# Performance work log

Measured on AMD Instinct MI355X. Metric: run time of the kernel, lower is better.

The kernel has to match this reference:

```python
import jax, jax.numpy as jnp
import numpy as np

N_ATOMS = 10000
N_PAIR = 100000
F = 128
N_HEAD = 4
FH = F // N_HEAD  # 32
DEGREES = [1, 2, 3]
N_DEG = len(DEGREES)
REPEATS = np.array([2 * l + 1 for l in DEGREES])  # [3,5,7]
M_TOT = int(REPEATS.sum())  # 15
K_RBF = 32


def ssp(x):
    # shifted softplus: softplus(x) - log(2)
    return jax.nn.softplus(x) - jnp.log(2.0).astype(x.dtype)


def setup_inputs() -> dict:
    key = jax.random.key(0)
    ks = jax.random.split(key, 16)
    inp = {
        "x": jax.random.normal(ks[0], (N_ATOMS, F), jnp.float32),
        "rbf_ij": jax.random.normal(ks[1], (N_PAIR, K_RBF), jnp.float32),
        "sph_ij": jax.random.normal(ks[2], (N_PAIR, M_TOT), jnp.float32),
        "phi_r_cut": jax.random.uniform(ks[3], (N_PAIR,), jnp.float32),
        "idx_i": jnp.sort(jax.random.randint(ks[4], (N_PAIR,), 0, N_ATOMS)),
        "idx_j": jax.random.randint(ks[5], (N_PAIR,), 0, N_ATOMS),
        "pair_mask": jnp.ones((N_PAIR,), jnp.float32),
        # params
        "W_Q": jax.random.normal(ks[6], (N_DEG, N_HEAD, FH, FH), jnp.float32) / np.sqrt(FH),
        "W_K": jax.random.normal(ks[7], (N_DEG, N_HEAD, FH, FH), jnp.float32) / np.sqrt(FH),
        # in2f MLP: single dense F -> F
        "W_in": jax.random.normal(ks[8], (F, F), jnp.float32) / np.sqrt(F),
        "b_in": jnp.zeros((F,), jnp.float32),
        # radial filter MLP: K -> K (ssp) -> n_deg*F
        "W_f1": jax.random.normal(ks[9], (K_RBF, K_RBF), jnp.float32) / np.sqrt(K_RBF),
        "b_f1": jnp.zeros((K_RBF,), jnp.float32),
        "W_f2": jax.random.normal(ks[10], (K_RBF, N_DEG * F), jnp.float32) / np.sqrt(K_RBF),
        "b_f2": jnp.zeros((N_DEG * F,), jnp.float32),
        # f2out MLP: single dense F -> F
        "W_out": jax.random.normal(ks[11], (F, F), jnp.float32) / np.sqrt(F),
        "b_out": jnp.zeros((F,), jnp.float32),
    }
    return inp


def reference(x, rbf_ij, sph_ij, phi_r_cut, idx_i, idx_j, pair_mask,
              W_Q, W_K, W_in, b_in, W_f1, b_f1, W_f2, b_f2, W_out, b_out):
    n = x.shape[0]
    # in2f embedding (last in2f dim == F)
    x_f = x @ W_in + b_in                                  # (n, F)
    x_head = x_f.reshape(n, N_HEAD, FH)                    # (n, h, FH)

    # per-degree, per-head linear maps (the nested vmap matmuls)
    Q = jnp.einsum('dhij,nhj->ndhi', W_Q, x_head)          # (n, n_deg, h, FH)
    K = jnp.einsum('dhij,nhj->ndhi', W_K, x_head)

    m = pair_mask[:, None, None, None]
    Q_i = Q[idx_i] * m                                     # (P, n_deg, h, FH)
    K_j = K[idx_j] * m

    # radial filter: MLP(rbf) -> (P, n_deg, h, FH), scaled by cutoff
    h1 = ssp(rbf_ij @ W_f1 + b_f1)
    W_ij = (h1 @ W_f2 + b_f2).reshape(-1, N_DEG, N_HEAD, FH)
    W_ij = W_ij * phi_r_cut[:, None, None, None]

    # attention coefficients per degree/head
    alpha = jnp.sum(Q_i * K_j * W_ij, axis=-1)             # (P, n_deg, h)
    alpha = jnp.repeat(alpha, repeats=REPEATS, axis=1, total_repeat_length=M_TOT)  # (P, m_tot, h)
    alpha = alpha / jnp.sqrt(jnp.asarray(FH, x.dtype))     # att_scale

    # outer product of neighbor features with spherical harmonics
    x_j = x_head[idx_j] * pair_mask[:, None, None]         # (P, h, FH)
    z_ij = jnp.einsum('pm,phf->pmhf', sph_ij, x_j)         # (P, m_tot, h, FH)
    z_ij = alpha[:, :, :, None] * z_ij
    z_ij = z_ij.reshape(z_ij.shape[0], M_TOT, F)           # (P, m_tot, F)

    agg = jax.ops.segment_sum(z_ij, idx_i, num_segments=n)  # (n, m_tot, F)

    # f2out projection (last f2out dim == F)
    out = agg @ W_out + b_out                               # (n, m_tot, F)
    return out
```

## Files before the change

kernel.cpp:

```cpp
#include <hip/hip_runtime.h>
#include <hip/hip_bf16.h>

#define N_ATOMS 10000
#define N_PAIR  100000
#define F_DIM   128
#define N_HEAD  4
#define FH      32
#define N_DEG   3
#define M_TOT   15
#define K_RBF   32
#define R_OUT   (N_ATOMS * M_TOT)
#define PPB     50

typedef __attribute__((ext_vector_type(8))) short short8;
typedef __attribute__((ext_vector_type(4))) float f32x4;

union frag_cast { int i[4]; short8 s; };

__device__ __forceinline__ float sspf(float v) {
    float sp = fmaxf(v, 0.f) + log1pf(expf(-fabsf(v)));
    return sp - 0.69314718055994531f;
}

__device__ __forceinline__ unsigned short bf16_rne(float x) {
    unsigned int u = __float_as_uint(x);
    unsigned int r = u + 0x7fffu + ((u >> 16) & 1u);
    return (unsigned short)(r >> 16);
}
__device__ __forceinline__ float bf16_tof(unsigned short h) {
    return __uint_as_float(((unsigned int)h) << 16);
}

__global__ __launch_bounds__(256) void k_binit(
    const float* __restrict__ b, float4* __restrict__ out, int n4)
{
    int i = blockIdx.x * 256 + threadIdx.x;
    int stride = gridDim.x * 256;
    for (; i < n4; i += stride) {
        int c4 = i & 31;
        out[i] = *(const float4*)(b + c4 * 4);
    }
}

__global__ __launch_bounds__(256) void k_gemm128(
    const float* __restrict__ A, const float* __restrict__ B,
    const float* __restrict__ bias, float* __restrict__ C, int rows)
{
    __shared__ float As[32][132];
    __shared__ float Bs[32][132];
    int r0 = blockIdx.x * 128;
    int t = threadIdx.x;
    int ty = t >> 4, tx = t & 15;

    float acc[8][8];
    #pragma unroll
    for (int i = 0; i < 8; ++i)
        #pragma unroll
        for (int j = 0; j < 8; ++j) acc[i][j] = 0.f;

    for (int k0 = 0; k0 < 128; k0 += 32) {
        #pragma unroll
        for (int r = 0; r < 16; ++r) {
            int idx = t + 256 * r;
            int row = idx >> 5, kk = idx & 31;
            int grow = r0 + row;
            As[kk][row] = (grow < rows) ? A[grow * 128 + k0 + kk] : 0.f;
        }
        #pragma unroll
        for (int r = 0; r < 16; ++r) {
            int idx = t + 256 * r;
            int kk = idx >> 7, c = idx & 127;
            Bs[kk][c] = B[(k0 + kk) * 128 + c];
        }
        __syncthreads();

        #pragma unroll
        for (int kk = 0; kk < 32; ++kk) {
            float a[8], b[8];
            *(float4*)&a[0] = *(const float4*)&As[kk][ty * 4];
            *(float4*)&a[4] = *(const float4*)&As[kk][64 + ty * 4];
            *(float4*)&b[0] = *(const float4*)&Bs[kk][tx * 4];
            *(float4*)&b[4] = *(const float4*)&Bs[kk][64 + tx * 4];
            #pragma unroll
            for (int i = 0; i < 8; ++i)
                #pragma unroll
                for (int j = 0; j < 8; ++j)
                    acc[i][j] = fmaf(a[i], b[j], acc[i][j]);
        }
        __syncthreads();
    }

    float bj[8];
    #pragma unroll
    for (int j = 0; j < 4; ++j) { bj[j] = bias[tx * 4 + j]; bj[4 + j] = bias[64 + tx * 4 + j]; }

    #pragma unroll
    for (int i = 0; i < 8; ++i) {
        int row = r0 + ((i < 4) ? (ty * 4 + i) : (64 + ty * 4 + (i - 4)));
        if (row < rows) {
            float4 v0, v1;
            v0.x = acc[i][0] + bj[0]; v0.y = acc[i][1] + bj[1];
            v0.z = acc[i][2] + bj[2]; v0.w = acc[i][3] + bj[3];
            v1.x = acc[i][4] + bj[4]; v1.y = acc[i][5] + bj[5];
            v1.z = acc[i][6] + bj[6]; v1.w = acc[i][7] + bj[7];
            *(float4*)&C[row * 128 + tx * 4] = v0;
            *(float4*)&C[row * 128 + 64 + tx * 4] = v1;
        }
    }
}

__global__ __launch_bounds__(384) void k_qk(
    const float* __restrict__ xh, const float* __restrict__ W_Q,
    const float* __restrict__ W_K, float* __restrict__ Q, float* __restrict__ K)
{
    __shared__ float xfs[32][128];
    int t = threadIdx.x;
    int h = (t >> 5) & 3;
    float wq[32], wk[32];
    const float4* wqp = (const float4*)(W_Q + t * 32);
    const float4* wkp = (const float4*)(W_K + t * 32);
    #pragma unroll
    for (int j4 = 0; j4 < 8; ++j4) {
        float4 a = wqp[j4], b = wkp[j4];
        wq[4 * j4 + 0] = a.x; wq[4 * j4 + 1] = a.y; wq[4 * j4 + 2] = a.z; wq[4 * j4 + 3] = a.w;
        wk[4 * j4 + 0] = b.x; wk[4 * j4 + 1] = b.y; wk[4 * j4 + 2] = b.z; wk[4 * j4 + 3] = b.w;
    }
    int ab = blockIdx.x * 32;
    for (int idx = t; idx < 4096; idx += 384) {
        int aa = idx >> 7, f = idx & 127;
        int ag = ab + aa;
        xfs[aa][f] = (ag < N_ATOMS) ? xh[ag * 128 + f] : 0.f;
    }
    __syncthreads();
    for (int aa = 0; aa < 32; ++aa) {
        int ag = ab + aa;
        if (ag >= N_ATOMS) break;
        const float4* xv = (const float4*)&xfs[aa][h * 32];
        float q0 = 0.f, q1 = 0.f, k0 = 0.f, k1 = 0.f;
        #pragma unroll
        for (int j4 = 0; j4 < 8; j4 += 2) {
            float4 x0 = xv[j4], x1 = xv[j4 + 1];
            q0 = fmaf(wq[4 * j4 + 0], x0.x, q0); q0 = fmaf(wq[4 * j4 + 1], x0.y, q0);
            q0 = fmaf(wq[4 * j4 + 2], x0.z, q0); q0 = fmaf(wq[4 * j4 + 3], x0.w, q0);
            q1 = fmaf(wq[4 * j4 + 4], x1.x, q1); q1 = fmaf(wq[4 * j4 + 5], x1.y, q1);
            q1 = fmaf(wq[4 * j4 + 6], x1.z, q1); q1 = fmaf(wq[4 * j4 + 7], x1.w, q1);
            k0 = fmaf(wk[4 * j4 + 0], x0.x, k0); k0 = fmaf(wk[4 * j4 + 1], x0.y, k0);
            k0 = fmaf(wk[4 * j4 + 2], x0.z, k0); k0 = fmaf(wk[4 * j4 + 3], x0.w, k0);
            k1 = fmaf(wk[4 * j4 + 4], x1.x, k1); k1 = fmaf(wk[4 * j4 + 5], x1.y, k1);
            k1 = fmaf(wk[4 * j4 + 6], x1.z, k1); k1 = fmaf(wk[4 * j4 + 7], x1.w, k1);
        }
        Q[ag * 384 + t] = q0 + q1;
        K[ag * 384 + t] = k0 + k1;
    }
}

__global__ __launch_bounds__(256) void k_cvt_w2(
    const float* __restrict__ W, unsigned short* __restrict__ Wh,
    unsigned short* __restrict__ Wl)
{
    int idx = blockIdx.x * 256 + threadIdx.x;
    if (idx < 12288) {
        int e = idx >> 5, k = idx & 31;
        float v = W[k * 384 + e];
        unsigned short h = bf16_rne(v);
        unsigned short l = bf16_rne(v - bf16_tof(h));
        Wh[e * 32 + k] = h;
        Wl[e * 32 + k] = l;
    }
}

__global__ __launch_bounds__(256) void k_pair(
    const float* __restrict__ rbf, const float* __restrict__ phi,
    const float* __restrict__ mask, const int* __restrict__ idx_i,
    const int* __restrict__ idx_j, const float* __restrict__ W_f1,
    const float* __restrict__ b_f1, const unsigned short* __restrict__ W2h,
    const unsigned short* __restrict__ W2l, const float* __restrict__ b_f2,
    const float* __restrict__ Q, const float* __restrict__ K,
    float* __restrict__ alpha)
{
    __shared__ float g_s[16][388];
    __shared__ unsigned int h1p_s[16][36];
    __shared__ int   i_s[16];
    __shared__ int   j_s[16];
    __shared__ float phim_s[16];

    float (*rbf_s)[33] = (float (*)[33])(&g_s[0][0]);
    float (*wf1_s)[33] = (float (*)[33])(&g_s[0][0] + 16 * 33);

    int t = threadIdx.x;
    int p0 = blockIdx.x * 16;

    for (int idx = t; idx < 1536; idx += 256) {
        if (idx < 512) {
            rbf_s[idx >> 5][idx & 31] = rbf[p0 * 32 + idx];
        } else {
            int k = idx - 512;
            wf1_s[k >> 5][k & 31] = W_f1[k];
        }
    }
    if (t < 16) {
        int pg = p0 + t;
        i_s[t] = idx_i[pg];
        j_s[t] = idx_j[pg];
        float m = mask[pg];
        phim_s[t] = phi[pg] * m * m * 0.17677669529663687f;
    }
    __syncthreads();

    {
        int p = t >> 4, c0 = (t & 15) * 2;
        float acc0 = b_f1[c0], acc1 = b_f1[c0 + 1];
        #pragma unroll
        for (int k = 0; k < 32; ++k) {
            float rv = rbf_s[p][k];
            acc0 = fmaf(rv, wf1_s[k][c0], acc0);
            acc1 = fmaf(rv, wf1_s[k][c0 + 1], acc1);
        }
        float h0 = sspf(acc0), h1v = sspf(acc1);
        unsigned short hh0 = bf16_rne(h0);
        unsigned short ll0 = bf16_rne(h0 - bf16_tof(hh0));
        unsigned short hh1 = bf16_rne(h1v);
        unsigned short ll1 = bf16_rne(h1v - bf16_tof(hh1));
        h1p_s[p][c0]     = ((unsigned int)hh0 << 16) | (unsigned int)ll0;
        h1p_s[p][c0 + 1] = ((unsigned int)hh1 << 16) | (unsigned int)ll1;
    }
    __syncthreads();

    #pragma unroll
    for (int it = 0; it < 6; ++it) {
        int idx = it * 256 + t;
        int p = idx / 96;
        int c4 = idx - p * 96;
        const float4* qp = (const float4*)(Q + i_s[p] * 384) + c4;
        const float4* kp = (const float4*)(K + j_s[p] * 384) + c4;
        float4 qv = *qp, kv = *kp;
        float4 gv;
        gv.x = qv.x * kv.x; gv.y = qv.y * kv.y;
        gv.z = qv.z * kv.z; gv.w = qv.w * kv.w;
        *(float4*)&g_s[p][c4 * 4] = gv;
    }
    __syncthreads();

    int wave = t >> 6, lane = t & 63;
    int quad = lane >> 4, l15 = lane & 15;

    short8 ah, al;
    {
        const unsigned int* hp = &h1p_s[l15][quad * 8];
        uint4 u01 = *(const uint4*)hp;
        uint4 u23 = *(const uint4*)(hp + 4);
        unsigned int u[8] = {u01.x, u01.y, u01.z, u01.w, u23.x, u23.y, u23.z, u23.w};
        frag_cast fh, fl;
        #pragma unroll
        for (int q = 0; q < 4; ++q) {
            unsigned int a0 = u[2 * q], a1 = u[2 * q + 1];
            fh.i[q] = (int)((a0 >> 16) | (a1 & 0xffff0000u));
            fl.i[q] = (int)((a0 & 0xffffu) | (a1 << 16));
        }
        ah = fh.s;
        al = fl.s;
    }

    #pragma unroll
    for (int dd = 0; dd < 3; ++dd) {
        int dh = wave * 3 + dd;
        int e_base = dh * 32;
        short8 bh0 = *(const short8*)(W2h + (e_base + l15) * 32 + quad * 8);
        short8 bl0 = *(const short8*)(W2l + (e_base + l15) * 32 + quad * 8);
        short8 bh1 = *(const short8*)(W2h + (e_base + 16 + l15) * 32 + quad * 8);
        short8 bl1 = *(const short8*)(W2l + (e_base + 16 + l15) * 32 + quad * 8);
        float b2v0 = b_f2[e_base + l15];
        float b2v1 = b_f2[e_base + 16 + l15];

        f32x4 s0 = {0.f, 0.f, 0.f, 0.f};
        f32x4 s1 = {0.f, 0.f, 0.f, 0.f};
        s0 = __builtin_amdgcn_mfma_f32_16x16x32_bf16(ah, bh0, s0, 0, 0, 0);
        s1 = __builtin_amdgcn_mfma_f32_16x16x32_bf16(ah, bh1, s1, 0, 0, 0);
        s0 = __builtin_amdgcn_mfma_f32_16x16x32_bf16(al, bh0, s0, 0, 0, 0);
        s1 = __builtin_amdgcn_mfma_f32_16x16x32_bf16(al, bh1, s1, 0, 0, 0);
        s0 = __builtin_amdgcn_mfma_f32_16x16x32_bf16(ah, bl0, s0, 0, 0, 0);
        s1 = __builtin_amdgcn_mfma_f32_16x16x32_bf16(ah, bl1, s1, 0, 0, 0);

        float vsum[4];
        #pragma unroll
        for (int r = 0; r < 4; ++r) {
            int prow = quad * 4 + r;
            float v = (s0[r] + b2v0) * g_s[prow][e_base + l15]
                    + (s1[r] + b2v1) * g_s[prow][e_base + 16 + l15];
            #pragma unroll
            for (int off = 8; off >= 1; off >>= 1)
                v += __shfl_xor(v, off, 16);
            vsum[r] = v;
        }
        if (l15 == 0) {
            #pragma unroll
            for (int r = 0; r < 4; ++r) {
                int prow = quad * 4 + r;
                alpha[(p0 + prow) * 12 + dh] = vsum[r] * phim_s[prow];
            }
        }
    }
}

__global__ __launch_bounds__(256) void k_xw(
    const float* __restrict__ xh, const float* __restrict__ W,
    float* __restrict__ xwh)
{
    __shared__ float xs[32][132];
    int t = threadIdx.x;
    int a0 = blockIdx.x * 32;
    #pragma unroll
    for (int it = 0; it < 4; ++it) {
        int idx = t + it * 256;
        int row = idx >> 5, c4 = (idx & 31) * 4;
        int ga = a0 + row;
        float4 v = make_float4(0.f, 0.f, 0.f, 0.f);
        if (ga < N_ATOMS) v = *(const float4*)(xh + ga * 128 + c4);
        *(float4*)&xs[row][c4] = v;
    }
    __syncthreads();

    int c = t & 127;
    int half = t >> 7;
    #pragma unroll
    for (int h = 0; h < 4; ++h) {
        float w[32];
        #pragma unroll
        for (int k = 0; k < 32; ++k) w[k] = W[(h * 32 + k) * 128 + c];
        float acc[16];
        #pragma unroll
        for (int i = 0; i < 16; ++i) acc[i] = 0.f;
        #pragma unroll
        for (int k = 0; k < 32; ++k) {
            float wv = w[k];
            #pragma unroll
            for (int i = 0; i < 16; ++i)
                acc[i] = fmaf(xs[half * 16 + i][h * 32 + k], wv, acc[i]);
        }
        #pragma unroll
        for (int i = 0; i < 16; ++i) {
            int ga = a0 + half * 16 + i;
            if (ga < N_ATOMS) xwh[(long)ga * 512 + h * 128 + c] = acc[i];
        }
    }
}

__device__ __forceinline__ void flush_acc(float* __restrict__ out, int a,
                                          const float* acc, float bout,
                                          int t, bool interior)
{
    float* base = out + (long)a * (M_TOT * 128) + t;
    if (interior) {
        #pragma unroll
        for (int m = 0; m < M_TOT; ++m) base[m * 128] = acc[m] + bout;
    } else {
        #pragma unroll
        for (int m = 0; m < M_TOT; ++m) atomicAdd(&base[m * 128], acc[m]);
    }
}

__global__ __launch_bounds__(512) void k_aggc(
    const float* __restrict__ xwh, const float* __restrict__ alpha,
    const float* __restrict__ sph, const int* __restrict__ idx_i,
    const int* __restrict__ idx_j, const float* __restrict__ mask,
    const float* __restrict__ b_out, float* __restrict__ out)
{
    int tid = threadIdx.x;
    int grp = tid >> 7;
    int t   = tid & 127;
    int g0  = (blockIdx.x * 4 + grp) * PPB;
    int g1  = g0 + PPB;

    float bout = b_out[t];
    int prevA = (g0 > 0) ? idx_i[g0 - 1] : -1;
    int nextA = (g1 < N_PAIR) ? idx_i[g1] : -1;

    float acc[M_TOT];
    #pragma unroll
    for (int m = 0; m < M_TOT; ++m) acc[m] = 0.f;

    int cur = idx_i[g0];
    bool started_inside = (cur != prevA);

    for (int p = g0; p < g1; ++p) {
        int ii = idx_i[p];
        if (ii != cur) {
            flush_acc(out, cur, acc, bout, t, started_inside);
            #pragma unroll
            for (int m = 0; m < M_TOT; ++m) acc[m] = 0.f;
            cur = ii;
            started_inside = true;
        }
        int jj = idx_j[p];
        const float* xp = xwh + (long)jj * 512;
        float xw0 = xp[t];
        float xw1 = xp[128 + t];
        float xw2 = xp[256 + t];
        float xw3 = xp[384 + t];
        float mv = mask[p];
        const float* ap = alpha + p * 12;
        float sd0 = (ap[0] * xw0 + ap[1] * xw1 + ap[2]  * xw2 + ap[3]  * xw3) * mv;
        float sd1 = (ap[4] * xw0 + ap[5] * xw1 + ap[6]  * xw2 + ap[7]  * xw3) * mv;
        float sd2 = (ap[8] * xw0 + ap[9] * xw1 + ap[10] * xw2 + ap[11] * xw3) * mv;
        const float* sp = sph + p * 15;
        #pragma unroll
        for (int m = 0; m < M_TOT; ++m) {
            float sdv = (m < 3) ? sd0 : ((m < 8) ? sd1 : sd2);
            acc[m] = fmaf(sp[m], sdv, acc[m]);
        }
    }
    bool interior = started_inside && (cur != nextA);
    flush_acc(out, cur, acc, bout, t, interior);
}

extern "C" void kernel_launch(void* const* d_in, const int* in_sizes, int n_in,
                              void* d_out, int out_size, void* d_ws, size_t ws_size,
                              hipStream_t stream) {
    const float* x        = (const float*)d_in[0];
    const float* rbf_ij   = (const float*)d_in[1];
    const float* sph_ij   = (const float*)d_in[2];
    const float* phi_r    = (const float*)d_in[3];
    const int*   idx_i    = (const int*)d_in[4];
    const int*   idx_j    = (const int*)d_in[5];
    const float* pmask    = (const float*)d_in[6];
    const float* W_Q      = (const float*)d_in[7];
    const float* W_K      = (const float*)d_in[8];
    const float* W_in     = (const float*)d_in[9];
    const float* b_in     = (const float*)d_in[10];
    const float* W_f1     = (const float*)d_in[11];
    const float* b_f1     = (const float*)d_in[12];
    const float* W_f2     = (const float*)d_in[13];
    const float* b_f2     = (const float*)d_in[14];
    const float* W_out    = (const float*)d_in[15];
    const float* b_out    = (const float*)d_in[16];
    float* out = (float*)d_out;

    float* ws    = (float*)d_ws;
    float* xh    = ws;
    float* Qbuf  = xh + N_ATOMS * F_DIM;
    float* Kbuf  = Qbuf + N_ATOMS * 384;
    float* alpha = Kbuf + N_ATOMS * 384;
    unsigned short* W2h = (unsigned short*)(alpha + N_PAIR * 12);
    unsigned short* W2l = W2h + 12288;
    float* xwh   = Qbuf;

    k_binit<<<2048, 256, 0, stream>>>(b_out, (float4*)d_out, R_OUT * 128 / 4);
    k_cvt_w2<<<48, 256, 0, stream>>>(W_f2, W2h, W2l);
    k_gemm128<<<(N_ATOMS + 127) / 128, 256, 0, stream>>>(x, W_in, b_in, xh, N_ATOMS);
    k_qk<<<(N_ATOMS + 31) / 32, 384, 0, stream>>>(xh, W_Q, W_K, Qbuf, Kbuf);
    k_pair<<<N_PAIR / 16, 256, 0, stream>>>(rbf_ij, phi_r, pmask, idx_i, idx_j,
                                            W_f1, b_f1, W2h, W2l, b_f2,
                                            Qbuf, Kbuf, alpha);
    k_xw<<<(N_ATOMS + 31) / 32, 256, 0, stream>>>(xh, W_out, xwh);
    k_aggc<<<N_PAIR / (4 * PPB), 512, 0, stream>>>(xwh, alpha, sph_ij, idx_i, idx_j,
                                                   pmask, b_out, out);
}
```

Baseline: 414.7 us.

## Store per-head xW table in fp16 interleaved and prefetch neighbor rows in aggregation

The k_xw output table now holds fp16 values with the four head values for each channel packed together, so k_aggc fetches one 8-byte ushort4 per pair instead of four strided fp32 loads. The aggregation loop software-prefetches the next neighbor's row and index one iteration ahead. PPB is halved so more blocks launch. This cuts gather bandwidth and latency at the cost of fp16 rounding on intermediate values and more boundary atomics from smaller segments.

New measurement: 719.4 us. +73.5%, slower.

```diff
diff --git a/kernel.cpp b/kernel.cpp
--- a/kernel.cpp
+++ b/kernel.cpp
@@ -10,12 +10,13 @@
 #define M_TOT   15
 #define K_RBF   32
 #define R_OUT   (N_ATOMS * M_TOT)
-#define PPB     50
+#define PPB     25
 
 typedef __attribute__((ext_vector_type(8))) short short8;
 typedef __attribute__((ext_vector_type(4))) float f32x4;
 
 union frag_cast { int i[4]; short8 s; };
+union h4u { ushort4 u; _Float16 h[4]; };
 
 __device__ __forceinline__ float sspf(float v) {
     float sp = fmaxf(v, 0.f) + log1pf(expf(-fabsf(v)));
@@ -304,7 +305,7 @@
 
 __global__ __launch_bounds__(256) void k_xw(
     const float* __restrict__ xh, const float* __restrict__ W,
-    float* __restrict__ xwh)
+    unsigned short* __restrict__ xwh)
 {
     __shared__ float xs[32][132];
     int t = threadIdx.x;
@@ -321,26 +322,31 @@
     __syncthreads();
 
     int c = t & 127;
-    int half = t >> 7;
+    int half_ = t >> 7;
+    float acc[4][16];
+    #pragma unroll
+    for (int h = 0; h < 4; ++h)
+        #pragma unroll
+        for (int i = 0; i < 16; ++i) acc[h][i] = 0.f;
+
     #pragma unroll
     for (int h = 0; h < 4; ++h) {
-        float w[32];
-        #pragma unroll
-        for (int k = 0; k < 32; ++k) w[k] = W[(h * 32 + k) * 128 + c];
-        float acc[16];
-        #pragma unroll
-        for (int i = 0; i < 16; ++i) acc[i] = 0.f;
         #pragma unroll
         for (int k = 0; k < 32; ++k) {
-            float wv = w[k];
+            float wv = W[(h * 32 + k) * 128 + c];
             #pragma unroll
             for (int i = 0; i < 16; ++i)
-                acc[i] = fmaf(xs[half * 16 + i][h * 32 + k], wv, acc[i]);
-        }
-        #pragma unroll
-        for (int i = 0; i < 16; ++i) {
-            int ga = a0 + half * 16 + i;
-            if (ga < N_ATOMS) xwh[(long)ga * 512 + h * 128 + c] = acc[i];
+                acc[h][i] = fmaf(xs[half_ * 16 + i][h * 32 + k], wv, acc[h][i]);
+        }
+    }
+    #pragma unroll
+    for (int i = 0; i < 16; ++i) {
+        int ga = a0 + half_ * 16 + i;
+        if (ga < N_ATOMS) {
+            h4u pk;
+            #pragma unroll
+            for (int h = 0; h < 4; ++h) pk.h[h] = (_Float16)acc[h][i];
+            *(ushort4*)(xwh + (long)ga * 512 + c * 4) = pk.u;
         }
     }
 }
@@ -360,11 +366,12 @@
 }
 
 __global__ __launch_bounds__(512) void k_aggc(
-    const float* __restrict__ xwh, const float* __restrict__ alpha,
+    const unsigned short* __restrict__ xwh, const float* __restrict__ alpha,
     const float* __restrict__ sph, const int* __restrict__ idx_i,
     const int* __restrict__ idx_j, const float* __restrict__ mask,
     const float* __restrict__ b_out, float* __restrict__ out)
 {
+    const ushort4* xwp = (const ushort4*)xwh;
     int tid = threadIdx.x;
     int grp = tid >> 7;
     int t   = tid & 127;
@@ -382,7 +389,17 @@
     int cur = idx_i[g0];
     bool started_inside = (cur != prevA);
 
+    int jc = idx_j[g0];
+    h4u xc; xc.u = xwp[(long)jc * 128 + t];
+    int jn = idx_j[g0 + 1];
+
     for (int p = g0; p < g1; ++p) {
+        h4u xn; xn.u = xc.u;
+        int jn2 = 0;
+        if (p + 1 < g1) {
+            xn.u = xwp[(long)jn * 128 + t];
+            if (p + 2 < g1) jn2 = idx_j[p + 2];
+        }
         int ii = idx_i[p];
         if (ii != cur) {
             flush_acc(out, cur, acc, bout, t, started_inside);
@@ -391,12 +408,10 @@
             cur = ii;
             started_inside = true;
         }
-        int jj = idx_j[p];
-        const float* xp = xwh + (long)jj * 512;
-        float xw0 = xp[t];
-        float xw1 = xp[128 + t];
-        float xw2 = xp[256 + t];
-        float xw3 = xp[384 + t];
+        float xw0 = (float)xc.h[0];
+        float xw1 = (float)xc.h[1];
+        float xw2 = (float)xc.h[2];
+        float xw3 = (float)xc.h[3];
         float mv = mask[p];
         const float* ap = alpha + p * 12;
         float sd0 = (ap[0] * xw0 + ap[1] * xw1 + ap[2]  * xw2 + ap[3]  * xw3) * mv;
@@ -408,6 +423,8 @@
             float sdv = (m < 3) ? sd0 : ((m < 8) ? sd1 : sd2);
             acc[m] = fmaf(sp[m], sdv, acc[m]);
         }
+        xc.u = xn.u;
+        jn = jn2;
     }
     bool interior = started_inside && (cur != nextA);
     flush_acc(out, cur, acc, bout, t, interior);
@@ -442,7 +459,7 @@
     float* alpha = Kbuf + N_ATOMS * 384;
     unsigned short* W2h = (unsigned short*)(alpha + N_PAIR * 12);
     unsigned short* W2l = W2h + 12288;
-    float* xwh   = Qbuf;
+    unsigned short* xwh = (unsigned short*)Qbuf;
 
     k_binit<<<2048, 256, 0, stream>>>(b_out, (float4*)d_out, R_OUT * 128 / 4);
     k_cvt_w2<<<48, 256, 0, stream>>>(W_f2, W2h, W2l);
```
